# Kernel optimization log

Hardware: AMD Instinct MI355X
Metric: run time of the kernel (lower is better)

The kernel has to match this reference:

```python
import jax, jax.numpy as jnp
import numpy as np

E, H, T_MAX = 1024, 16, 2048
HS = E // H
EPS = 1e-5


def _layernorm(x, g, b):
    m = jnp.mean(x, axis=-1, keepdims=True)
    v = jnp.mean(jnp.square(x - m), axis=-1, keepdims=True)
    return (x - m) * jax.lax.rsqrt(v + EPS) * g + b


def setup_inputs() -> dict:
    key = jax.random.key(0)
    ks = jax.random.split(key, 8)
    B, T = 2, 2048
    s = 0.02
    return {
        "x": jax.random.normal(ks[0], (B, T, E), jnp.float32),
        "ln1_g": jnp.ones((E,), jnp.float32),
        "ln1_b": jnp.zeros((E,), jnp.float32),
        "Wk": jax.random.normal(ks[1], (H, E, HS), jnp.float32) * s,  # stacked per-head key weights (x @ Wk)
        "Wv": jax.random.normal(ks[2], (H, E, HS), jnp.float32) * s,
        "Wproj": jax.random.normal(ks[3], (E, E), jnp.float32) * s,
        "bproj": jnp.zeros((E,), jnp.float32),
        "ln2_g": jnp.ones((E,), jnp.float32),
        "ln2_b": jnp.zeros((E,), jnp.float32),
        "W1": jax.random.normal(ks[4], (E, 4 * E), jnp.float32) * s,
        "b1": jnp.zeros((4 * E,), jnp.float32),
        "W2": jax.random.normal(ks[5], (4 * E, E), jnp.float32) * s,
        "b2": jnp.zeros((E,), jnp.float32),
    }


def reference(x, ln1_g, ln1_b, Wk, Wv, Wproj, bproj, ln2_g, ln2_b, W1, b1, W2, b2):
    B, T, C = x.shape
    h = _layernorm(x, ln1_g, ln1_b)
    # NOTE: original code uses the KEY projection for both q and k (q = self.key(x))
    k = jnp.einsum('bte,hed->bhtd', h, Wk)
    q = k
    wei = jnp.einsum('bhtd,bhsd->bhts', q, k) * (C ** -0.5)  # scale by full n_embd, as in source
    causal = jnp.tril(jnp.ones((T, T), bool))
    wei = jnp.where(causal, wei, -jnp.inf)
    # source applies softmax over dim=1 (the query/row axis of the TxT matrix)
    wei = jax.nn.softmax(wei, axis=2)
    v = jnp.einsum('bte,hed->bhtd', h, Wv)
    attn = jnp.einsum('bhts,bhsd->bhtd', wei, v)          # [B,H,T,HS]
    attn = attn.transpose(0, 2, 1, 3).reshape(B, T, C)    # concat heads
    x = x + attn @ Wproj + bproj
    h2 = _layernorm(x, ln2_g, ln2_b)
    x = x + jax.nn.relu(h2 @ W1 + b1) @ W2 + b2
    return x
```

## Files before the change

kernel.cpp:

```cpp
#include <hip/hip_runtime.h>

using bf16x8 = __attribute__((ext_vector_type(8))) __bf16;
using f32x4  = __attribute__((ext_vector_type(4))) float;

__device__ __forceinline__ f32x4 mfma16(bf16x8 a, bf16x8 b, f32x4 c) {
  return __builtin_amdgcn_mfma_f32_16x16x32_bf16(a, b, c, 0, 0, 0);
}

__device__ __forceinline__ unsigned short f2bf(float f) {
  union { float f; unsigned int u; } x; x.f = f;
  unsigned int u = x.u + 0x7FFFu + ((x.u >> 16) & 1u);
  return (unsigned short)(u >> 16);
}

__device__ __forceinline__ unsigned int cvtpk_bf16(float lo, float hi) {
  unsigned int r;
  asm("v_cvt_pk_bf16_f32 %0, %1, %2" : "=v"(r) : "v"(lo), "v"(hi));
  return r;
}

__device__ __forceinline__ void gl_lds16(const unsigned short* g, unsigned short* l) {
  __builtin_amdgcn_global_load_lds(
      (__attribute__((address_space(1))) void*)(g),
      (__attribute__((address_space(3))) void*)(l), 16, 0, 0);
}

__global__ __launch_bounds__(256) void transpose_cvt(const float* __restrict__ in,
                                                     unsigned short* __restrict__ out,
                                                     int R, int C) {
  __shared__ float t[32][33];
  int b = blockIdx.z;
  const float* inb = in + (size_t)b * R * C;
  unsigned short* outb = out + (size_t)b * R * C;
  int tx = threadIdx.x & 31, ty = threadIdx.x >> 5;
  int c0 = blockIdx.x * 32, r0 = blockIdx.y * 32;
#pragma unroll
  for (int i = 0; i < 4; ++i)
    t[ty + i * 8][tx] = inb[(size_t)(r0 + ty + i * 8) * C + c0 + tx];
  __syncthreads();
#pragma unroll
  for (int i = 0; i < 4; ++i)
    outb[(size_t)(c0 + ty + i * 8) * R + r0 + tx] = f2bf(t[tx][ty + i * 8]);
}

__global__ __launch_bounds__(256) void ln_bf16(const float* __restrict__ x,
                                               const float* __restrict__ g,
                                               const float* __restrict__ bta,
                                               unsigned short* __restrict__ out) {
  int row = blockIdx.x, tid = threadIdx.x;
  float4 v = reinterpret_cast<const float4*>(x + (size_t)row * 1024)[tid];
  float s = v.x + v.y + v.z + v.w;
  float s2 = v.x * v.x + v.y * v.y + v.z * v.z + v.w * v.w;
#pragma unroll
  for (int m = 1; m < 64; m <<= 1) { s += __shfl_xor(s, m); s2 += __shfl_xor(s2, m); }
  __shared__ float red[8];
  int w = tid >> 6;
  if ((tid & 63) == 0) { red[w] = s; red[w + 4] = s2; }
  __syncthreads();
  s  = red[0] + red[1] + red[2] + red[3];
  s2 = red[4] + red[5] + red[6] + red[7];
  float mean = s * (1.f / 1024.f);
  float var  = s2 * (1.f / 1024.f) - mean * mean;
  float rstd = rsqrtf(var + 1e-5f);
  float4 gv = reinterpret_cast<const float4*>(g)[tid];
  float4 bv = reinterpret_cast<const float4*>(bta)[tid];
  ushort4 o;
  o.x = f2bf((v.x - mean) * rstd * gv.x + bv.x);
  o.y = f2bf((v.y - mean) * rstd * gv.y + bv.y);
  o.z = f2bf((v.z - mean) * rstd * gv.z + bv.z);
  o.w = f2bf((v.w - mean) * rstd * gv.w + bv.w);
  reinterpret_cast<ushort4*>(out + (size_t)row * 1024)[tid] = o;
}

__device__ __forceinline__ void stage_half(const unsigned short* gbase, int K,
                                           unsigned short* lds, int tid) {
#pragma unroll
  for (int j = 0; j < 2; ++j) {
    int lr = j * 64 + (tid >> 3);
    int c  = (tid & 7) ^ (lr & 7);
    gl_lds16(gbase + (size_t)lr * K + c * 8, lds + (size_t)(j * 512 + tid) * 8);
  }
}

__device__ __forceinline__ bf16x8 rdfrag(const unsigned short* base, int r, int k) {
  return *reinterpret_cast<const bf16x8*>(base + ((size_t)r * 8 + (k ^ (r & 7))) * 8);
}

__global__ __launch_bounds__(512, 2) void gemm256_relu(const unsigned short* __restrict__ A,
                                                       const unsigned short* __restrict__ Bt,
                                                       unsigned short* __restrict__ C,
                                                       const float* __restrict__ bias,
                                                       int M, int N, int K) {
  __shared__ __align__(16) unsigned short LA[2][256 * 64];
  __shared__ __align__(16) unsigned short LB[2][256 * 64];
  int tid = threadIdx.x, lane = tid & 63, w = tid >> 6;
  int l15 = lane & 15, lh = lane >> 4;
  int wr = (w >> 2) * 128, wc = (w & 3) * 64;
  int bid = blockIdx.x;
  int xcd = bid & 7, g = bid >> 3;
  int bm = (xcd >> 1) * 4 + (g >> 3);
  int bn = (xcd & 1) * 8 + (g & 7);
  const unsigned short* Ab = A + (size_t)(bm * 256) * K;
  const unsigned short* Bb = Bt + (size_t)(bn * 256) * K;
  f32x4 acc[8][4] = {};
  int NT = K >> 6;
  stage_half(Ab, K, &LA[0][0], tid);
  stage_half(Ab + (size_t)128 * K, K, &LA[0][128 * 64], tid);
  stage_half(Bb, K, &LB[0][0], tid);
  stage_half(Bb + (size_t)128 * K, K, &LB[0][128 * 64], tid);
  asm volatile("s_waitcnt vmcnt(0)" ::: "memory");
  __builtin_amdgcn_s_barrier();
  for (int t = 0; t < NT; ++t) {
    int cur = t & 1;
    const unsigned short* la = &LA[cur][0];
    const unsigned short* lb = &LB[cur][0];
    unsigned short* na = &LA[cur ^ 1][0];
    unsigned short* nb = &LB[cur ^ 1][0];
    int k0n = (t + 1) << 6;
    bool more = (t + 1 < NT);
    bf16x8 bfr[4][2];
#pragma unroll
    for (int q = 0; q < 4; ++q) {
      if (more) {
        if (q == 0)      stage_half(Ab + k0n, K, na, tid);
        else if (q == 1) stage_half(Ab + (size_t)128 * K + k0n, K, na + 128 * 64, tid);
        else if (q == 2) stage_half(Bb + k0n, K, nb, tid);
        else             stage_half(Bb + (size_t)128 * K + k0n, K, nb + 128 * 64, tid);
      }
      if (q == 0) {
        if (more) asm volatile("s_waitcnt vmcnt(2)" ::: "memory");
        else      asm volatile("s_waitcnt vmcnt(0)" ::: "memory");
        __builtin_amdgcn_s_barrier();
      }
      bf16x8 aq[2][2];
#pragma unroll
      for (int i = 0; i < 2; ++i)
#pragma unroll
        for (int kk = 0; kk < 2; ++kk)
          aq[i][kk] = rdfrag(la, wr + q * 32 + i * 16 + l15, kk * 4 + lh);
      if (q == 0) {
#pragma unroll
        for (int ni = 0; ni < 4; ++ni)
#pragma unroll
          for (int kk = 0; kk < 2; ++kk)
            bfr[ni][kk] = rdfrag(lb, wc + ni * 16 + l15, kk * 4 + lh);
      }
      if (q != 0) __builtin_amdgcn_s_barrier();
      __builtin_amdgcn_s_setprio(1);
#pragma unroll
      for (int kk = 0; kk < 2; ++kk)
#pragma unroll
        for (int i = 0; i < 2; ++i)
#pragma unroll
          for (int ni = 0; ni < 4; ++ni)
            acc[q * 2 + i][ni] = mfma16(aq[i][kk], bfr[ni][kk], acc[q * 2 + i][ni]);
      __builtin_amdgcn_s_setprio(0);
      __builtin_amdgcn_s_barrier();
    }
  }
#pragma unroll
  for (int mi = 0; mi < 8; ++mi)
#pragma unroll
    for (int ni = 0; ni < 4; ++ni) {
      int row0 = bm * 256 + wr + mi * 16 + lh * 4;
      int col  = bn * 256 + wc + ni * 16 + l15;
      float bv = bias[col];
#pragma unroll
      for (int r = 0; r < 4; ++r) {
        float v = fmaxf(acc[mi][ni][r] + bv, 0.f);
        C[(size_t)(row0 + r) * N + col] = f2bf(v);
      }
    }
}

#define GBK 128
#define KSCL 0.04508422f

__device__ __forceinline__ bf16x8 rd128(const unsigned short* base, int r, int ch) {
  int c = ch ^ ((r & 7) << 1);
  return *reinterpret_cast<const bf16x8*>(base + (size_t)r * GBK + c * 8);
}

template<int TM, int MODE>
__global__ __launch_bounds__(256) void gemm_bf16(const unsigned short* __restrict__ A,
                                                 const unsigned short* __restrict__ Bt,
                                                 void* __restrict__ Cout,
                                                 unsigned short* __restrict__ Cout2,
                                                 const float* __restrict__ bias,
                                                 const float* __restrict__ resid,
                                                 const float* __restrict__ scvec,
                                                 int M, int N, int K) {
  constexpr int MI = TM / 32;
  constexpr int AJ = TM / 16;
  __shared__ __align__(16) unsigned short Sh[(TM + 128) * GBK];
  unsigned short* As = Sh;
  unsigned short* Bs = Sh + TM * GBK;
  int tid = threadIdx.x;
  int lane = tid & 63, w = tid >> 6;
  int l15 = lane & 15, lh = lane >> 4;
  int wr = (w >> 1) * (TM / 2), wc = (w & 1) * 64;
  int nblk = N >> 7;
  int rows = M / TM;
  int bm, bn;
  if (nblk == 8 && (rows & 7) == 0) {
    int bid = blockIdx.x;
    int xcd = bid & 7, g = bid >> 3;
    bm = xcd * (rows >> 3) + (g >> 3);
    bn = g & 7;
  } else {
    bm = blockIdx.x / nblk; bn = blockIdx.x % nblk;
  }
  const unsigned short* ApJ[AJ];
  const unsigned short* BpJ[8];
#pragma unroll
  for (int j = 0; j < AJ; ++j) {
    int row = j * 16 + (tid >> 4);
    int ch  = (tid & 15) ^ ((row & 7) << 1);
    ApJ[j] = A + (size_t)(bm * TM + row) * K + ch * 8;
  }
#pragma unroll
  for (int j = 0; j < 8; ++j) {
    int row = j * 16 + (tid >> 4);
    int ch  = (tid & 15) ^ ((row & 7) << 1);
    BpJ[j] = Bt + (size_t)(bn * 128 + row) * K + ch * 8;
  }
  f32x4 acc[MI][4] = {};
  for (int k0 = 0; k0 < K; k0 += GBK) {
#pragma unroll
    for (int j = 0; j < AJ; ++j)
      gl_lds16(ApJ[j] + k0, &As[(j * 256 + tid) * 8]);
#pragma unroll
    for (int j = 0; j < 8; ++j)
      gl_lds16(BpJ[j] + k0, &Bs[(j * 256 + tid) * 8]);
    __syncthreads();
    bf16x8 af[MI][4], bfr[4][4];
#pragma unroll
    for (int i = 0; i < MI; ++i)
#pragma unroll
      for (int kk = 0; kk < 4; ++kk)
        af[i][kk] = rd128(As, wr + i * 16 + l15, kk * 4 + lh);
#pragma unroll
    for (int i = 0; i < 4; ++i)
#pragma unroll
      for (int kk = 0; kk < 4; ++kk)
        bfr[i][kk] = rd128(Bs, wc + i * 16 + l15, kk * 4 + lh);
#pragma unroll
    for (int kk = 0; kk < 4; ++kk)
#pragma unroll
      for (int mi = 0; mi < MI; ++mi)
#pragma unroll
        for (int ni = 0; ni < 4; ++ni)
          acc[mi][ni] = mfma16(af[mi][kk], bfr[ni][kk], acc[mi][ni]);
    __syncthreads();
  }
  if constexpr (MODE == 3) {
#pragma unroll
    for (int mi = 0; mi < MI; ++mi) {
#pragma unroll
      for (int ni = 0; ni < 4; ++ni) {
        int tl = wr + mi * 16 + lh * 4;
        int dl = wc + ni * 16 + l15;
        int colg = bn * 128 + dl;
        int bb = bm >> 5, hh = colg >> 6;
        const float* sp = scvec + (size_t)(bb * 16 + hh) * 2048 + (bm & 31) * 64 + tl;
        float4 rs = *reinterpret_cast<const float4*>(sp);
        unsigned int p0 = f2bf(acc[mi][ni][0] * rs.x) | ((unsigned int)f2bf(acc[mi][ni][1] * rs.y) << 16);
        unsigned int p1 = f2bf(acc[mi][ni][2] * rs.z) | ((unsigned int)f2bf(acc[mi][ni][3] * rs.w) << 16);
        uint2 pk = {p0, p1};
        *reinterpret_cast<uint2*>(&Sh[dl * 64 + (tl ^ ((dl & 7) << 3))]) = pk;
      }
    }
    __syncthreads();
    int dr = tid >> 1, th = (tid & 1) * 32;
    int bb = bm >> 5, tbase = (bm & 31) * 64;
    size_t colg = bn * 128 + dr;
    unsigned short* Vt = (unsigned short*)Cout;
#pragma unroll
    for (int j = 0; j < 4; ++j) {
      int t = th + j * 8;
      int4 v = *reinterpret_cast<const int4*>(&Sh[dr * 64 + (t ^ ((dr & 7) << 3))]);
      *reinterpret_cast<int4*>(&Vt[((size_t)bb * 1024 + colg) * 2048 + tbase + t]) = v;
    }
  } else {
#pragma unroll
    for (int mi = 0; mi < MI; ++mi) {
#pragma unroll
      for (int ni = 0; ni < 4; ++ni) {
        int row0 = bm * TM + wr + mi * 16 + lh * 4;
        int col  = bn * 128 + wc + ni * 16 + l15;
        float bv = (MODE == 2) ? 0.f : bias[col];
#pragma unroll
        for (int r = 0; r < 4; ++r) {
          int row = row0 + r;
          float v = acc[mi][ni][r] + bv;
          if constexpr (MODE == 0) {
            v += resid[(size_t)row * N + col];
            ((float*)Cout)[(size_t)row * N + col] = v;
          } else {
            ((unsigned short*)Cout)[(size_t)row * N + col] = f2bf(v);
            Cout2[(size_t)row * N + col] = f2bf(v * KSCL);
          }
        }
      }
    }
  }
}

__device__ __forceinline__ int comp_map(int q, int x) {
  return (q < 2) ? (q * 8 + x) : (31 - ((q - 2) * 8 + x));
}

__global__ __launch_bounds__(256) void attn_stats(const unsigned short* __restrict__ Kb,
                                                  const unsigned short* __restrict__ Kbs,
                                                  float* __restrict__ colrcp) {
  __shared__ __align__(16) unsigned short Kt[2][64][72];
  int bid = blockIdx.x;
  int q = bid >> 8, r8 = bid & 255;
  int x = r8 >> 5, bh = r8 & 31;
  int b = bh >> 4, h = bh & 15;
  int sb = comp_map(q, x);
  int tid = threadIdx.x, lane = tid & 63, w = tid >> 6;
  int l15 = lane & 15, lh = lane >> 4;
  int s0 = sb * 64;
  const unsigned short* Kp  = Kb  + ((size_t)b * 2048) * 1024 + h * 64;
  const unsigned short* Kps = Kbs + ((size_t)b * 2048) * 1024 + h * 64;
  bf16x8 as[2];
#pragma unroll
  for (int kc = 0; kc < 2; ++kc)
    as[kc] = *reinterpret_cast<const bf16x8*>(Kp + (size_t)(s0 + w * 16 + l15) * 1024 + kc * 32 + (lh << 3));
  int r0 = tid >> 3, c0 = (tid & 7) << 3;
  int4 g0 = *reinterpret_cast<const int4*>(Kps + (size_t)(s0 + r0) * 1024 + c0);
  int4 g1 = *reinterpret_cast<const int4*>(Kps + (size_t)(s0 + 32 + r0) * 1024 + c0);
  *reinterpret_cast<int4*>(&Kt[0][r0][c0]) = g0;
  *reinterpret_cast<int4*>(&Kt[0][32 + r0][c0]) = g1;
  float l[4] = {0.f, 0.f, 0.f, 0.f};
  int nt = 32 - sb;
  for (int it = 0; it < nt; ++it) {
    int t0 = s0 + it * 64;
    int cur = it & 1;
    if (it + 1 < nt) {
      g0 = *reinterpret_cast<const int4*>(Kps + (size_t)(t0 + 64 + r0) * 1024 + c0);
      g1 = *reinterpret_cast<const int4*>(Kps + (size_t)(t0 + 96 + r0) * 1024 + c0);
    }
    __syncthreads();
#pragma unroll
    for (int tf = 0; tf < 4; ++tf) {
      bf16x8 bt0 = *reinterpret_cast<const bf16x8*>(&Kt[cur][tf * 16 + l15][lh << 3]);
      bf16x8 bt1 = *reinterpret_cast<const bf16x8*>(&Kt[cur][tf * 16 + l15][32 + (lh << 3)]);
      f32x4 z = {};
      f32x4 sa = mfma16(as[1], bt1, mfma16(as[0], bt0, z));
      int tg = t0 + tf * 16 + l15;
#pragma unroll
      for (int r = 0; r < 4; ++r) {
        float e = exp2f(sa[r]);
        if (it == 0) { int sg = s0 + w * 16 + lh * 4 + r; e = (tg >= sg) ? e : 0.f; }
        l[r] += e;
      }
    }
    if (it + 1 < nt) {
      *reinterpret_cast<int4*>(&Kt[cur ^ 1][r0][c0]) = g0;
      *reinterpret_cast<int4*>(&Kt[cur ^ 1][32 + r0][c0]) = g1;
    }
  }
#pragma unroll
  for (int m = 1; m < 16; m <<= 1)
#pragma unroll
    for (int r = 0; r < 4; ++r)
      l[r] += __shfl_xor(l[r], m);
  if (l15 == 0) {
#pragma unroll
    for (int r = 0; r < 4; ++r)
      colrcp[(size_t)bh * 2048 + s0 + w * 16 + lh * 4 + r] = 1.f / l[r];
  }
}

__global__ __launch_bounds__(256) void attn_pv(const unsigned short* __restrict__ Kb,
                                               const unsigned short* __restrict__ Kbs,
                                               const unsigned short* __restrict__ Vt,
                                               unsigned short* __restrict__ attn) {
  __shared__ __align__(16) unsigned short Ks[2][64][72];
  __shared__ __align__(16) unsigned short Pl[4][16][72];
  int bid = blockIdx.x;
  int q = bid >> 8, r8 = bid & 255;
  int x = r8 >> 5, bh = r8 & 31;
  int b = bh >> 4, h = bh & 15;
  int tb = comp_map(q, x);
  int tid = threadIdx.x, lane = tid & 63, w = tid >> 6;
  int l15 = lane & 15, lh = lane >> 4;
  int t0 = tb * 64;
  const unsigned short* Kp  = Kb  + ((size_t)b * 2048) * 1024 + h * 64;
  const unsigned short* Kps = Kbs + ((size_t)b * 2048) * 1024 + h * 64;
  const unsigned short* Vp  = Vt + (size_t)bh * 64 * 2048;
  bf16x8 at[2];
#pragma unroll
  for (int kc = 0; kc < 2; ++kc)
    at[kc] = *reinterpret_cast<const bf16x8*>(Kp + (size_t)(t0 + w * 16 + l15) * 1024 + kc * 32 + (lh << 3));
  int r0 = tid >> 3, c0 = (tid & 7) << 3;
  int4 g0 = *reinterpret_cast<const int4*>(Kps + (size_t)r0 * 1024 + c0);
  int4 g1 = *reinterpret_cast<const int4*>(Kps + (size_t)(32 + r0) * 1024 + c0);
  *reinterpret_cast<int4*>(&Ks[0][r0][c0]) = g0;
  *reinterpret_cast<int4*>(&Ks[0][32 + r0][c0]) = g1;
  f32x4 acc[4] = {};
  int nt = tb + 1;
  for (int it = 0; it < nt; ++it) {
    int s0 = it * 64;
    int cur = it & 1;
    bf16x8 va[2][4];
#pragma unroll
    for (int c2 = 0; c2 < 2; ++c2)
#pragma unroll
      for (int nf = 0; nf < 4; ++nf)
        va[c2][nf] = *reinterpret_cast<const bf16x8*>(Vp + (size_t)(nf * 16 + l15) * 2048 + s0 + c2 * 32 + (lh << 3));
    if (it + 1 < nt) {
      g0 = *reinterpret_cast<const int4*>(Kps + (size_t)(s0 + 64 + r0) * 1024 + c0);
      g1 = *reinterpret_cast<const int4*>(Kps + (size_t)(s0 + 96 + r0) * 1024 + c0);
    }
    __syncthreads();
    bool diag = (it == nt - 1);
#pragma unroll
    for (int sf = 0; sf < 4; ++sf) {
      bf16x8 ks0 = *reinterpret_cast<const bf16x8*>(&Ks[cur][sf * 16 + l15][lh << 3]);
      bf16x8 ks1 = *reinterpret_cast<const bf16x8*>(&Ks[cur][sf * 16 + l15][32 + (lh << 3)]);
      f32x4 z = {};
      f32x4 sa = mfma16(ks1, at[1], mfma16(ks0, at[0], z));
      float pe[4];
#pragma unroll
      for (int r = 0; r < 4; ++r) {
        float p = exp2f(sa[r]);
        if (diag) {
          int sg = s0 + sf * 16 + lh * 4 + r;
          int tg = t0 + w * 16 + l15;
          p = (sg <= tg) ? p : 0.f;
        }
        pe[r] = p;
      }
      unsigned int u0 = cvtpk_bf16(pe[0], pe[1]);
      unsigned int u1 = cvtpk_bf16(pe[2], pe[3]);
      unsigned long long pk = (unsigned long long)u0 | ((unsigned long long)u1 << 32);
      *reinterpret_cast<unsigned long long*>(&Pl[w][l15][sf * 16 + lh * 4]) = pk;
    }
#pragma unroll
    for (int c2 = 0; c2 < 2; ++c2) {
      bf16x8 pa = *reinterpret_cast<const bf16x8*>(&Pl[w][l15][c2 * 32 + (lh << 3)]);
#pragma unroll
      for (int nf = 0; nf < 4; ++nf)
        acc[nf] = mfma16(pa, va[c2][nf], acc[nf]);
    }
    if (it + 1 < nt) {
      *reinterpret_cast<int4*>(&Ks[cur ^ 1][r0][c0]) = g0;
      *reinterpret_cast<int4*>(&Ks[cur ^ 1][32 + r0][c0]) = g1;
    }
  }
#pragma unroll
  for (int nf = 0; nf < 4; ++nf)
#pragma unroll
    for (int r = 0; r < 4; ++r) {
      int t = t0 + w * 16 + lh * 4 + r;
      attn[(size_t)(b * 2048 + t) * 1024 + h * 64 + nf * 16 + l15] = f2bf(acc[nf][r]);
    }
}

extern "C" void kernel_launch(void* const* d_in, const int* in_sizes, int n_in,
                              void* d_out, int out_size, void* d_ws, size_t ws_size,
                              hipStream_t stream) {
  (void)in_sizes; (void)n_in; (void)out_size; (void)ws_size;
  const float* x     = (const float*)d_in[0];
  const float* ln1_g = (const float*)d_in[1];
  const float* ln1_b = (const float*)d_in[2];
  const float* Wk    = (const float*)d_in[3];
  const float* Wv    = (const float*)d_in[4];
  const float* Wproj = (const float*)d_in[5];
  const float* bproj = (const float*)d_in[6];
  const float* ln2_g = (const float*)d_in[7];
  const float* ln2_b = (const float*)d_in[8];
  const float* W1    = (const float*)d_in[9];
  const float* b1    = (const float*)d_in[10];
  const float* W2    = (const float*)d_in[11];
  const float* b2    = (const float*)d_in[12];
  float* out = (float*)d_out;

  char* ws = (char*)d_ws;
  size_t off = 0;
  auto alloc = [&](size_t bytes) { void* p = ws + off; off += (bytes + 255) & ~(size_t)255; return p; };
  unsigned short* bufA = (unsigned short*)alloc((size_t)4096 * 1024 * 2);
  unsigned short* wk_t = (unsigned short*)alloc((size_t)1024 * 1024 * 2);
  unsigned short* wv_t = (unsigned short*)alloc((size_t)1024 * 1024 * 2);
  unsigned short* wp_t = (unsigned short*)alloc((size_t)1024 * 1024 * 2);
  unsigned short* w1_t = (unsigned short*)alloc((size_t)1024 * 4096 * 2);
  unsigned short* w2_t = (unsigned short*)alloc((size_t)4096 * 1024 * 2);
  unsigned short* Kb   = (unsigned short*)alloc((size_t)4096 * 1024 * 2);
  unsigned short* Kbs  = (unsigned short*)alloc((size_t)4096 * 1024 * 2);
  unsigned short* Vt   = (unsigned short*)alloc((size_t)4096 * 1024 * 2);
  float* colrcp = (float*)alloc((size_t)32 * 2048 * 4);
  float* y      = (float*)alloc((size_t)4096 * 1024 * 4);
  unsigned short* act = (unsigned short*)alloc((size_t)4096 * 4096 * 2);

  dim3 b256(256);
  transpose_cvt<<<dim3(2, 32, 16), b256, 0, stream>>>(Wk, wk_t, 1024, 64);
  transpose_cvt<<<dim3(2, 32, 16), b256, 0, stream>>>(Wv, wv_t, 1024, 64);
  transpose_cvt<<<dim3(32, 32, 1), b256, 0, stream>>>(Wproj, wp_t, 1024, 1024);
  transpose_cvt<<<dim3(128, 32, 1), b256, 0, stream>>>(W1, w1_t, 1024, 4096);
  transpose_cvt<<<dim3(32, 128, 1), b256, 0, stream>>>(W2, w2_t, 4096, 1024);

  ln_bf16<<<4096, b256, 0, stream>>>(x, ln1_g, ln1_b, bufA);
  gemm_bf16<64, 2><<<512, b256, 0, stream>>>(bufA, wk_t, Kb, Kbs, nullptr, nullptr, nullptr, 4096, 1024, 1024);
  attn_stats<<<1024, b256, 0, stream>>>(Kb, Kbs, colrcp);
  gemm_bf16<64, 3><<<512, b256, 0, stream>>>(bufA, wv_t, Vt, nullptr, nullptr, nullptr, colrcp, 4096, 1024, 1024);
  attn_pv<<<1024, b256, 0, stream>>>(Kb, Kbs, Vt, bufA);
  gemm_bf16<64, 0><<<512, b256, 0, stream>>>(bufA, wp_t, y, nullptr, bproj, x, nullptr, 4096, 1024, 1024);
  ln_bf16<<<4096, b256, 0, stream>>>(y, ln2_g, ln2_b, bufA);
  gemm256_relu<<<256, dim3(512), 0, stream>>>(bufA, w1_t, act, b1, 4096, 4096, 1024);
  gemm_bf16<64, 0><<<512, b256, 0, stream>>>(act, w2_t, out, nullptr, b2, y, nullptr, 4096, 1024, 4096);
}
```

Before: 262.8 us.

## Enlarge attention tiles to 128 rows with direct-to-LDS swizzled K/V staging

```diff
diff --git a/kernel.cpp b/kernel.cpp
--- a/kernel.cpp
+++ b/kernel.cpp
@@ -23,6 +23,11 @@
   __builtin_amdgcn_global_load_lds(
       (__attribute__((address_space(1))) void*)(g),
       (__attribute__((address_space(3))) void*)(l), 16, 0, 0);
+}
+
+__device__ __forceinline__ bf16x8 rdsw64(const unsigned short* base, int r, int ch) {
+  int c = ch ^ (r & 7);
+  return *reinterpret_cast<const bf16x8*>(base + ((size_t)r * 8 + c) * 8);
 }
 
 __global__ __launch_bounds__(256) void transpose_cvt(const float* __restrict__ in,
@@ -306,61 +311,54 @@
   }
 }
 
-__device__ __forceinline__ int comp_map(int q, int x) {
-  return (q < 2) ? (q * 8 + x) : (31 - ((q - 2) * 8 + x));
-}
-
-__global__ __launch_bounds__(256) void attn_stats(const unsigned short* __restrict__ Kb,
+__global__ __launch_bounds__(512) void attn_stats(const unsigned short* __restrict__ Kb,
                                                   const unsigned short* __restrict__ Kbs,
                                                   float* __restrict__ colrcp) {
-  __shared__ __align__(16) unsigned short Kt[2][64][72];
+  __shared__ __align__(16) unsigned short Kt[2][64 * 64];
   int bid = blockIdx.x;
-  int q = bid >> 8, r8 = bid & 255;
-  int x = r8 >> 5, bh = r8 & 31;
+  int q = bid >> 8, x = (bid >> 5) & 7, bh = bid & 31;
   int b = bh >> 4, h = bh & 15;
-  int sb = comp_map(q, x);
+  int sb = q ? (15 - x) : x;
   int tid = threadIdx.x, lane = tid & 63, w = tid >> 6;
   int l15 = lane & 15, lh = lane >> 4;
-  int s0 = sb * 64;
+  int s0 = sb * 128, sw = s0 + w * 16;
   const unsigned short* Kp  = Kb  + ((size_t)b * 2048) * 1024 + h * 64;
   const unsigned short* Kps = Kbs + ((size_t)b * 2048) * 1024 + h * 64;
   bf16x8 as[2];
 #pragma unroll
   for (int kc = 0; kc < 2; ++kc)
-    as[kc] = *reinterpret_cast<const bf16x8*>(Kp + (size_t)(s0 + w * 16 + l15) * 1024 + kc * 32 + (lh << 3));
-  int r0 = tid >> 3, c0 = (tid & 7) << 3;
-  int4 g0 = *reinterpret_cast<const int4*>(Kps + (size_t)(s0 + r0) * 1024 + c0);
-  int4 g1 = *reinterpret_cast<const int4*>(Kps + (size_t)(s0 + 32 + r0) * 1024 + c0);
-  *reinterpret_cast<int4*>(&Kt[0][r0][c0]) = g0;
-  *reinterpret_cast<int4*>(&Kt[0][32 + r0][c0]) = g1;
+    as[kc] = *reinterpret_cast<const bf16x8*>(Kp + (size_t)(sw + l15) * 1024 + kc * 32 + (lh << 3));
+  int srow = tid >> 3;
+  int sch  = (tid & 7) ^ (srow & 7);
+  const unsigned short* ksrc = Kps + (size_t)srow * 1024 + sch * 8;
+  gl_lds16(ksrc + (size_t)s0 * 1024, &Kt[0][tid * 8]);
+  __syncthreads();
   float l[4] = {0.f, 0.f, 0.f, 0.f};
-  int nt = 32 - sb;
+  int nt = 32 - 2 * sb;
   for (int it = 0; it < nt; ++it) {
     int t0 = s0 + it * 64;
     int cur = it & 1;
-    if (it + 1 < nt) {
-      g0 = *reinterpret_cast<const int4*>(Kps + (size_t)(t0 + 64 + r0) * 1024 + c0);
-      g1 = *reinterpret_cast<const int4*>(Kps + (size_t)(t0 + 96 + r0) * 1024 + c0);
+    if (it + 1 < nt)
+      gl_lds16(ksrc + (size_t)(t0 + 64) * 1024, &Kt[cur ^ 1][tid * 8]);
+    if (t0 + 63 >= sw) {
+      bool dmask = (t0 < sw + 16);
+#pragma unroll
+      for (int tf = 0; tf < 4; ++tf) {
+        int tr = tf * 16 + l15;
+        bf16x8 bt0 = rdsw64(&Kt[cur][0], tr, lh);
+        bf16x8 bt1 = rdsw64(&Kt[cur][0], tr, 4 + lh);
+        f32x4 z = {};
+        f32x4 sa = mfma16(as[1], bt1, mfma16(as[0], bt0, z));
+        int tg = t0 + tr;
+#pragma unroll
+        for (int r = 0; r < 4; ++r) {
+          float e = exp2f(sa[r]);
+          if (dmask) { int sg = sw + lh * 4 + r; e = (tg >= sg) ? e : 0.f; }
+          l[r] += e;
+        }
+      }
     }
     __syncthreads();
-#pragma unroll
-    for (int tf = 0; tf < 4; ++tf) {
-      bf16x8 bt0 = *reinterpret_cast<const bf16x8*>(&Kt[cur][tf * 16 + l15][lh << 3]);
-      bf16x8 bt1 = *reinterpret_cast<const bf16x8*>(&Kt[cur][tf * 16 + l15][32 + (lh << 3)]);
-      f32x4 z = {};
-      f32x4 sa = mfma16(as[1], bt1, mfma16(as[0], bt0, z));
-      int tg = t0 + tf * 16 + l15;
-#pragma unroll
-      for (int r = 0; r < 4; ++r) {
-        float e = exp2f(sa[r]);
-        if (it == 0) { int sg = s0 + w * 16 + lh * 4 + r; e = (tg >= sg) ? e : 0.f; }
-        l[r] += e;
-      }
-    }
-    if (it + 1 < nt) {
-      *reinterpret_cast<int4*>(&Kt[cur ^ 1][r0][c0]) = g0;
-      *reinterpret_cast<int4*>(&Kt[cur ^ 1][32 + r0][c0]) = g1;
-    }
   }
 #pragma unroll
   for (int m = 1; m < 16; m <<= 1)
@@ -370,92 +368,90 @@
   if (l15 == 0) {
 #pragma unroll
     for (int r = 0; r < 4; ++r)
-      colrcp[(size_t)bh * 2048 + s0 + w * 16 + lh * 4 + r] = 1.f / l[r];
-  }
-}
-
-__global__ __launch_bounds__(256) void attn_pv(const unsigned short* __restrict__ Kb,
+      colrcp[(size_t)bh * 2048 + sw + lh * 4 + r] = 1.f / l[r];
+  }
+}
+
+__global__ __launch_bounds__(512) void attn_pv(const unsigned short* __restrict__ Kb,
                                                const unsigned short* __restrict__ Kbs,
                                                const unsigned short* __restrict__ Vt,
                                                unsigned short* __restrict__ attn) {
-  __shared__ __align__(16) unsigned short Ks[2][64][72];
-  __shared__ __align__(16) unsigned short Pl[4][16][72];
+  __shared__ __align__(16) unsigned short Ks[2][64 * 64];
+  __shared__ __align__(16) unsigned short Vs[2][64 * 64];
+  __shared__ __align__(16) unsigned short Pl[8][16][68];
   int bid = blockIdx.x;
-  int q = bid >> 8, r8 = bid & 255;
-  int x = r8 >> 5, bh = r8 & 31;
+  int q = bid >> 8, x = (bid >> 5) & 7, bh = bid & 31;
   int b = bh >> 4, h = bh & 15;
-  int tb = comp_map(q, x);
+  int tb = q ? (15 - x) : x;
   int tid = threadIdx.x, lane = tid & 63, w = tid >> 6;
   int l15 = lane & 15, lh = lane >> 4;
-  int t0 = tb * 64;
+  int t0 = tb * 128, tw = t0 + w * 16;
   const unsigned short* Kp  = Kb  + ((size_t)b * 2048) * 1024 + h * 64;
   const unsigned short* Kps = Kbs + ((size_t)b * 2048) * 1024 + h * 64;
   const unsigned short* Vp  = Vt + (size_t)bh * 64 * 2048;
   bf16x8 at[2];
 #pragma unroll
   for (int kc = 0; kc < 2; ++kc)
-    at[kc] = *reinterpret_cast<const bf16x8*>(Kp + (size_t)(t0 + w * 16 + l15) * 1024 + kc * 32 + (lh << 3));
-  int r0 = tid >> 3, c0 = (tid & 7) << 3;
-  int4 g0 = *reinterpret_cast<const int4*>(Kps + (size_t)r0 * 1024 + c0);
-  int4 g1 = *reinterpret_cast<const int4*>(Kps + (size_t)(32 + r0) * 1024 + c0);
-  *reinterpret_cast<int4*>(&Ks[0][r0][c0]) = g0;
-  *reinterpret_cast<int4*>(&Ks[0][32 + r0][c0]) = g1;
+    at[kc] = *reinterpret_cast<const bf16x8*>(Kp + (size_t)(tw + l15) * 1024 + kc * 32 + (lh << 3));
+  int srow = tid >> 3;
+  int sch  = (tid & 7) ^ (srow & 7);
+  const unsigned short* ksrc = Kps + (size_t)srow * 1024 + sch * 8;
+  const unsigned short* vsrc = Vp + (size_t)srow * 2048 + sch * 8;
+  gl_lds16(ksrc, &Ks[0][tid * 8]);
+  gl_lds16(vsrc, &Vs[0][tid * 8]);
+  __syncthreads();
   f32x4 acc[4] = {};
-  int nt = tb + 1;
+  int nt = 2 * tb + 2;
   for (int it = 0; it < nt; ++it) {
     int s0 = it * 64;
     int cur = it & 1;
-    bf16x8 va[2][4];
-#pragma unroll
-    for (int c2 = 0; c2 < 2; ++c2)
-#pragma unroll
-      for (int nf = 0; nf < 4; ++nf)
-        va[c2][nf] = *reinterpret_cast<const bf16x8*>(Vp + (size_t)(nf * 16 + l15) * 2048 + s0 + c2 * 32 + (lh << 3));
     if (it + 1 < nt) {
-      g0 = *reinterpret_cast<const int4*>(Kps + (size_t)(s0 + 64 + r0) * 1024 + c0);
-      g1 = *reinterpret_cast<const int4*>(Kps + (size_t)(s0 + 96 + r0) * 1024 + c0);
+      gl_lds16(ksrc + (size_t)(s0 + 64) * 1024, &Ks[cur ^ 1][tid * 8]);
+      gl_lds16(vsrc + (s0 + 64), &Vs[cur ^ 1][tid * 8]);
+    }
+    if (s0 <= tw + 15) {
+      bool dmask = (s0 + 63 > tw);
+#pragma unroll
+      for (int sf = 0; sf < 4; ++sf) {
+        int sr = sf * 16 + l15;
+        bf16x8 ks0 = rdsw64(&Ks[cur][0], sr, lh);
+        bf16x8 ks1 = rdsw64(&Ks[cur][0], sr, 4 + lh);
+        f32x4 z = {};
+        f32x4 sa = mfma16(ks1, at[1], mfma16(ks0, at[0], z));
+        float pe[4];
+#pragma unroll
+        for (int r = 0; r < 4; ++r) {
+          float p = exp2f(sa[r]);
+          if (dmask) {
+            int sg = s0 + sf * 16 + lh * 4 + r;
+            int tg = tw + l15;
+            p = (sg <= tg) ? p : 0.f;
+          }
+          pe[r] = p;
+        }
+        unsigned int u0 = cvtpk_bf16(pe[0], pe[1]);
+        unsigned int u1 = cvtpk_bf16(pe[2], pe[3]);
+        unsigned long long pk = (unsigned long long)u0 | ((unsigned long long)u1 << 32);
+        *reinterpret_cast<unsigned long long*>(&Pl[w][l15][sf * 16 + lh * 4]) = pk;
+      }
+#pragma unroll
+      for (int c2 = 0; c2 < 2; ++c2) {
+        bf16x8 pa = *reinterpret_cast<const bf16x8*>(&Pl[w][l15][c2 * 32 + (lh << 3)]);
+#pragma unroll
+        for (int nf = 0; nf < 4; ++nf) {
+          int dr = nf * 16 + l15;
+          bf16x8 vb = rdsw64(&Vs[cur][0], dr, c2 * 4 + lh);
+          acc[nf] = mfma16(pa, vb, acc[nf]);
+        }
+      }
     }
     __syncthreads();
-    bool diag = (it == nt - 1);
-#pragma unroll
-    for (int sf = 0; sf < 4; ++sf) {
-      bf16x8 ks0 = *reinterpret_cast<const bf16x8*>(&Ks[cur][sf * 16 + l15][lh << 3]);
-      bf16x8 ks1 = *reinterpret_cast<const bf16x8*>(&Ks[cur][sf * 16 + l15][32 + (lh << 3)]);
-      f32x4 z = {};
-      f32x4 sa = mfma16(ks1, at[1], mfma16(ks0, at[0], z));
-      float pe[4];
-#pragma unroll
-      for (int r = 0; r < 4; ++r) {
-        float p = exp2f(sa[r]);
-        if (diag) {
-          int sg = s0 + sf * 16 + lh * 4 + r;
-          int tg = t0 + w * 16 + l15;
-          p = (sg <= tg) ? p : 0.f;
-        }
-        pe[r] = p;
-      }
-      unsigned int u0 = cvtpk_bf16(pe[0], pe[1]);
-      unsigned int u1 = cvtpk_bf16(pe[2], pe[3]);
-      unsigned long long pk = (unsigned long long)u0 | ((unsigned long long)u1 << 32);
-      *reinterpret_cast<unsigned long long*>(&Pl[w][l15][sf * 16 + lh * 4]) = pk;
-    }
-#pragma unroll
-    for (int c2 = 0; c2 < 2; ++c2) {
-      bf16x8 pa = *reinterpret_cast<const bf16x8*>(&Pl[w][l15][c2 * 32 + (lh << 3)]);
-#pragma unroll
-      for (int nf = 0; nf < 4; ++nf)
-        acc[nf] = mfma16(pa, va[c2][nf], acc[nf]);
-    }
-    if (it + 1 < nt) {
-      *reinterpret_cast<int4*>(&Ks[cur ^ 1][r0][c0]) = g0;
-      *reinterpret_cast<int4*>(&Ks[cur ^ 1][32 + r0][c0]) = g1;
-    }
   }
 #pragma unroll
   for (int nf = 0; nf < 4; ++nf)
 #pragma unroll
     for (int r = 0; r < 4; ++r) {
-      int t = t0 + w * 16 + lh * 4 + r;
+      int t = tw + lh * 4 + r;
       attn[(size_t)(b * 2048 + t) * 1024 + h * 64 + nf * 16 + l15] = f2bf(acc[nf][r]);
     }
 }
@@ -495,7 +491,7 @@
   float* y      = (float*)alloc((size_t)4096 * 1024 * 4);
   unsigned short* act = (unsigned short*)alloc((size_t)4096 * 4096 * 2);
 
-  dim3 b256(256);
+  dim3 b256(256), b512(512);
   transpose_cvt<<<dim3(2, 32, 16), b256, 0, stream>>>(Wk, wk_t, 1024, 64);
   transpose_cvt<<<dim3(2, 32, 16), b256, 0, stream>>>(Wv, wv_t, 1024, 64);
   transpose_cvt<<<dim3(32, 32, 1), b256, 0, stream>>>(Wproj, wp_t, 1024, 1024);
@@ -504,9 +500,9 @@
 
   ln_bf16<<<4096, b256, 0, stream>>>(x, ln1_g, ln1_b, bufA);
   gemm_bf16<64, 2><<<512, b256, 0, stream>>>(bufA, wk_t, Kb, Kbs, nullptr, nullptr, nullptr, 4096, 1024, 1024);
-  attn_stats<<<1024, b256, 0, stream>>>(Kb, Kbs, colrcp);
+  attn_stats<<<512, b512, 0, stream>>>(Kb, Kbs, colrcp);
   gemm_bf16<64, 3><<<512, b256, 0, stream>>>(bufA, wv_t, Vt, nullptr, nullptr, nullptr, colrcp, 4096, 1024, 1024);
-  attn_pv<<<1024, b256, 0, stream>>>(Kb, Kbs, Vt, bufA);
+  attn_pv<<<512, b512, 0, stream>>>(Kb, Kbs, Vt, bufA);
   gemm_bf16<64, 0><<<512, b256, 0, stream>>>(bufA, wp_t, y, nullptr, bproj, x, nullptr, 4096, 1024, 1024);
   ln_bf16<<<4096, b256, 0, stream>>>(y, ln2_g, ln2_b, bufA);
   gemm256_relu<<<256, dim3(512), 0, stream>>>(bufA, w1_t, act, b1, 4096, 4096, 1024);
```

Measured after the change: 252.2 us. 4.0% less time.
